# Kernel optimization log

Measured on AMD Instinct MI355X. Metric: run time of the kernel, lower is better.

Reference implementation:

```python
import jax, jax.numpy as jnp
import numpy as np
from jax import lax

B, T, E = 2, 2048, 2048
H, D = 16, 128
C = H * D          # qk_dim == v_dim == 2048
K = 4              # short conv kernel size
EPS = 1e-5


def setup_inputs() -> dict:
    key = jax.random.key(0)
    ks = jax.random.split(key, 11)
    s = 0.02
    return {
        "x": jax.random.normal(ks[0], (B, T, E), dtype=jnp.float32),
        "recurrent_state": jnp.zeros((B, H, D, D), dtype=jnp.float32),
        "Wq": jax.random.normal(ks[1], (C, E), dtype=jnp.float32) * s,
        "Wk": jax.random.normal(ks[2], (C, E), dtype=jnp.float32) * s,
        "Wv": jax.random.normal(ks[3], (C, E), dtype=jnp.float32) * s,
        "Wbeta": jax.random.normal(ks[4], (H, E), dtype=jnp.float32) * s,
        "Wgate": jax.random.normal(ks[5], (C, E), dtype=jnp.float32) * s,
        "Wo": jax.random.normal(ks[6], (E, C), dtype=jnp.float32) * s,
        "wq_conv": jax.random.normal(ks[7], (C, 1, K), dtype=jnp.float32) * 0.5,
        "wk_conv": jax.random.normal(ks[8], (C, 1, K), dtype=jnp.float32) * 0.5,
        "wv_conv": jax.random.normal(ks[9], (C, 1, K), dtype=jnp.float32) * 0.5,
    }


def _causal_dwconv(u, w):
    # u: (B, T, C), w: (C, 1, K). Torch pads both sides by K-1 then truncates
    # to length T -> equivalent to causal left-pad of K-1.
    u = u.transpose(0, 2, 1)  # (B, C, T)
    y = lax.conv_general_dilated(
        u, w, window_strides=(1,), padding=[(K - 1, 0)],
        feature_group_count=C, dimension_numbers=("NCH", "OIH", "NCH"))
    return y.transpose(0, 2, 1)  # (B, T, C)


def _delta_scan(q, k, v, beta, state):
    # q,k,v: (B,T,H,D); beta: (B,T,H); state: (B,H,D,D)
    def step(S, inp):
        qt, kt, vt, bt = inp  # (B,H,D),(B,H,D),(B,H,D),(B,H)
        b = bt[..., None, None]
        S = (1.0 - b) * S + b * (kt[..., :, None] * vt[..., None, :])  # bhde
        o = jnp.einsum("bhde,bhd->bhe", S, qt)
        return S, o

    xs = (q.transpose(1, 0, 2, 3), k.transpose(1, 0, 2, 3),
          v.transpose(1, 0, 2, 3), beta.transpose(1, 0, 2))
    final_state, outs = lax.scan(step, state, xs)
    return outs.transpose(1, 0, 2, 3), final_state  # (B,T,H,D)


def reference(x, recurrent_state, Wq, Wk, Wv, Wbeta, Wgate, Wo,
              wq_conv, wk_conv, wv_conv):
    q = jax.nn.silu(_causal_dwconv(x @ Wq.T, wq_conv))
    k = jax.nn.silu(_causal_dwconv(x @ Wk.T, wk_conv))
    v = jax.nn.silu(_causal_dwconv(x @ Wv.T, wv_conv))
    beta = jax.nn.sigmoid(x @ Wbeta.T)   # (B,T,H)
    gate = jax.nn.sigmoid(x @ Wgate.T)   # (B,T,C)

    q = q.reshape(B, T, H, D) * (D ** -0.5)
    k = k.reshape(B, T, H, D)
    v = v.reshape(B, T, H, D)

    out, new_state = _delta_scan(q, k, v, beta, recurrent_state)  # (B,T,H,D)

    # GroupNorm(num_groups=H, channels=C, affine=False) over (B, C, T):
    # normalizes each (batch, head) group over its (D, T) elements.
    mean = out.mean(axis=(1, 3), keepdims=True)
    var = out.var(axis=(1, 3), keepdims=True)
    out = (out - mean) * lax.rsqrt(var + EPS)

    out = out.reshape(B, T, C) * gate
    y = out @ Wo.T  # (B,T,E)
    return y, new_state
```

## Files before the change

### kernel.cpp

```cpp
#include <hip/hip_runtime.h>
#include <hip/hip_bf16.h>
#include <math.h>

#define BB 2
#define TT 2048
#define EE 2048
#define HH 16
#define DD 128
#define CC 2048
#define KCONV 4
#define CHUNK 128
#define NC 16
#define GN_EPS 1e-5f

typedef __bf16 bf16x8 __attribute__((ext_vector_type(8)));
typedef __bf16 bf16x4 __attribute__((ext_vector_type(4)));
typedef float  f32x4  __attribute__((ext_vector_type(4)));

#define GLD16(gp, lp)                                                          \
  __builtin_amdgcn_global_load_lds(                                            \
      (const __attribute__((address_space(1))) void*)(gp),                     \
      (__attribute__((address_space(3))) void*)(lp), 16, 0, 0)

__device__ __forceinline__ bf16x8 ldfrag(const __bf16* buf, int row, int kg)
{
  return *(const bf16x8*)(buf + row * 128 + ((kg ^ (row & 7)) << 3));
}

__global__ __launch_bounds__(256)
void convert_all(const float* __restrict__ x,  const float* __restrict__ Wq,
                 const float* __restrict__ Wk, const float* __restrict__ Wv,
                 const float* __restrict__ Wg, const float* __restrict__ Wo,
                 __bf16* __restrict__ xbf, __bf16* __restrict__ Wcat,
                 __bf16* __restrict__ Wob)
{
  const int i = (blockIdx.x * 256 + threadIdx.x) * 4;
  const int XN = 8388608, WN = 4194304;
  const float* src;
  __bf16* dst;
  int off;
  if (i < XN) { src = x; dst = xbf; off = i; }
  else if (i < XN + 4 * WN) {
    const int j = i - XN;
    const int seg = j >> 22;
    src = seg == 0 ? Wq : seg == 1 ? Wk : seg == 2 ? Wv : Wg;
    dst = Wcat + ((size_t)seg << 22);
    off = j & (WN - 1);
  } else { src = Wo; dst = Wob; off = i - XN - 4 * WN; }
  const float4 v = *(const float4*)(src + off);
  bf16x4 o;
  o[0] = (__bf16)v.x; o[1] = (__bf16)v.y; o[2] = (__bf16)v.z; o[3] = (__bf16)v.w;
  *(bf16x4*)(dst + off) = o;
}

__global__ __launch_bounds__(256)
void beta_ker(const float* __restrict__ x, const float* __restrict__ Wb,
              float* __restrict__ betab)
{
  __shared__ float wsb[16 * 1024];
  const int tid = threadIdx.x;
  const int w = tid >> 6, lane = tid & 63;
  const int row = blockIdx.x * 4 + w;
  const float* xrow = x + (size_t)row * EE;

  float acc[16] = {};
#pragma unroll
  for (int kt = 0; kt < 2; ++kt) {
    __syncthreads();
#pragma unroll
    for (int it = 0; it < 16; ++it) {
      const int i = tid + it * 256;
      const int h = i >> 8, kq = i & 255;
      *(float4*)&wsb[h * 1024 + kq * 4] =
          *(const float4*)(Wb + (size_t)h * EE + kt * 1024 + kq * 4);
    }
    __syncthreads();
#pragma unroll
    for (int j = 0; j < 4; ++j) {
      const int kof = lane * 4 + j * 256;
      const float4 xv = *(const float4*)(xrow + kt * 1024 + kof);
#pragma unroll
      for (int h = 0; h < 16; ++h) {
        const float4 wv = *(const float4*)&wsb[h * 1024 + kof];
        acc[h] += xv.x * wv.x + xv.y * wv.y + xv.z * wv.z + xv.w * wv.w;
      }
    }
  }
#pragma unroll
  for (int h = 0; h < 16; ++h) {
#pragma unroll
    for (int off = 32; off; off >>= 1)
      acc[h] += __shfl_xor(acc[h], off, 64);
  }
#pragma unroll
  for (int h = 0; h < 16; ++h)
    if (lane == h)
      betab[(size_t)row * HH + h] = 1.f / (1.f + expf(-acc[h]));
}

__global__ __launch_bounds__(512)
void gemm_big(const __bf16* __restrict__ A, const __bf16* __restrict__ Bm,
              __bf16* __restrict__ o0, __bf16* __restrict__ o1,
              __bf16* __restrict__ o2, __bf16* __restrict__ o3)
{
  __shared__ __attribute__((aligned(16))) unsigned char smem[163840];
  __bf16 (*ldsA)[256 * 64] = (__bf16(*)[256 * 64])smem;
  __bf16 (*ldsB)[256 * 64] = (__bf16(*)[256 * 64])(smem + 98304);

  const int tid = threadIdx.x;
  const int w = tid >> 6, l = tid & 63;
  const int wm = w >> 2, wn = w & 3;
  const int m0 = blockIdx.y * 256, n0 = blockIdx.x * 256;
  const int NT = EE / 64;

  const int sr0 = w * 8 + (l >> 3);
  const int skg = l & 7;
  const int fr = l & 15;
  const int fkg = l >> 4;

#define STAGE_A(tile, half) do {                                               \
    const int b_ = (tile) % 3;                                                 \
    const int r0_ = sr0;                                                       \
    const int r1_ = 64 + sr0;                                                  \
    GLD16(A + (size_t)(m0 + (half) * 128 + r0_) * 2048 + (tile) * 64           \
              + ((skg ^ (r0_ & 7)) << 3),                                      \
          ldsA[b_] + ((half) * 128 + w * 8) * 64);                             \
    GLD16(A + (size_t)(m0 + (half) * 128 + r1_) * 2048 + (tile) * 64           \
              + ((skg ^ (r1_ & 7)) << 3),                                      \
          ldsA[b_] + ((half) * 128 + 64 + w * 8) * 64);                        \
  } while (0)

#define STAGE_B(tile, half) do {                                               \
    const int b_ = (tile) & 1;                                                 \
    const int r0_ = sr0;                                                       \
    const int r1_ = 64 + sr0;                                                  \
    GLD16(Bm + (size_t)(n0 + (half) * 128 + r0_) * 2048 + (tile) * 64          \
              + ((skg ^ (r0_ & 7)) << 3),                                      \
          ldsB[b_] + ((half) * 128 + w * 8) * 64);                             \
    GLD16(Bm + (size_t)(n0 + (half) * 128 + r1_) * 2048 + (tile) * 64          \
              + ((skg ^ (r1_ & 7)) << 3),                                      \
          ldsB[b_] + ((half) * 128 + 64 + w * 8) * 64);                        \
  } while (0)

#define LDA_FRAG(dst, ab, q, mf, ks) do {                                      \
    const int row_ = wm * 128 + (q) * 32 + (mf) * 16 + fr;                     \
    const int kg_ = (ks) * 4 + fkg;                                            \
    dst = *(const bf16x8*)&ldsA[ab][row_ * 64 + ((kg_ ^ (row_ & 7)) << 3)];    \
  } while (0)
#define LDB_FRAG(dst, bb, nf, ks) do {                                         \
    const int row_ = wn * 64 + (nf) * 16 + fr;                                 \
    const int kg_ = (ks) * 4 + fkg;                                            \
    dst = *(const bf16x8*)&ldsB[bb][row_ * 64 + ((kg_ ^ (row_ & 7)) << 3)];    \
  } while (0)

  f32x4 acc[8][4] = {};

  STAGE_A(0, 0); STAGE_A(0, 1); STAGE_B(0, 0); STAGE_B(0, 1);
  STAGE_A(1, 0); STAGE_A(1, 1); STAGE_B(1, 0);
  asm volatile("s_waitcnt vmcnt(6)" ::: "memory");
  __builtin_amdgcn_s_barrier();

  for (int t = 0; t < NT; ++t) {
    const int abuf = t % 3;
    const int bbuf = t & 1;
    bf16x8 bfr[4][2];

    {
#pragma unroll
      for (int nf = 0; nf < 4; ++nf)
#pragma unroll
        for (int ks = 0; ks < 2; ++ks) LDB_FRAG(bfr[nf][ks], bbuf, nf, ks);
      bf16x8 af[2][2];
#pragma unroll
      for (int mf = 0; mf < 2; ++mf)
#pragma unroll
        for (int ks = 0; ks < 2; ++ks) LDA_FRAG(af[mf][ks], abuf, 0, mf, ks);
      if (t + 1 < NT) STAGE_B(t + 1, 1);
      __builtin_amdgcn_s_barrier();
      __builtin_amdgcn_s_setprio(1);
#pragma unroll
      for (int mf = 0; mf < 2; ++mf)
#pragma unroll
        for (int nf = 0; nf < 4; ++nf)
#pragma unroll
          for (int ks = 0; ks < 2; ++ks)
            acc[mf][nf] = __builtin_amdgcn_mfma_f32_16x16x32_bf16(
                af[mf][ks], bfr[nf][ks], acc[mf][nf], 0, 0, 0);
      __builtin_amdgcn_s_setprio(0);
    }

#pragma unroll
    for (int q = 1; q < 4; ++q) {
      bf16x8 af[2][2];
#pragma unroll
      for (int mf = 0; mf < 2; ++mf)
#pragma unroll
        for (int ks = 0; ks < 2; ++ks) LDA_FRAG(af[mf][ks], abuf, q, mf, ks);
      if (q == 1) {
        if (t + 2 < NT) STAGE_A(t + 2, 0);
      } else if (q == 2) {
        if (t + 2 < NT) STAGE_A(t + 2, 1);
      } else {
        if (t + 2 < NT) STAGE_B(t + 2, 0);
        if (t == NT - 2)     asm volatile("s_waitcnt vmcnt(0)" ::: "memory");
        else if (t < NT - 2) asm volatile("s_waitcnt vmcnt(6)" ::: "memory");
      }
      __builtin_amdgcn_s_barrier();
      __builtin_amdgcn_s_setprio(1);
#pragma unroll
      for (int mf = 0; mf < 2; ++mf)
#pragma unroll
        for (int nf = 0; nf < 4; ++nf)
#pragma unroll
          for (int ks = 0; ks < 2; ++ks)
            acc[2 * q + mf][nf] = __builtin_amdgcn_mfma_f32_16x16x32_bf16(
                af[mf][ks], bfr[nf][ks], acc[2 * q + mf][nf], 0, 0, 0);
      __builtin_amdgcn_s_setprio(0);
    }
  }

  __syncthreads();
  const int proj = n0 >> 11;
  const int nb = n0 & 2047;
  __bf16* outp = proj == 0 ? o0 : proj == 1 ? o1 : proj == 2 ? o2 : o3;
  __bf16* ep = (__bf16*)smem + (size_t)w * 9216;
  const int crow = (l >> 4) * 4;
#pragma unroll
  for (int mf2 = 0; mf2 < 8; ++mf2)
#pragma unroll
    for (int nf = 0; nf < 4; ++nf)
#pragma unroll
      for (int r = 0; r < 4; ++r) {
        const int row = mf2 * 16 + crow + r;
        float vv = acc[mf2][nf][r];
        if (proj == 3) vv = 1.f / (1.f + expf(-vv));
        ep[row * 72 + nf * 16 + fr] = (__bf16)vv;
      }
#pragma unroll
  for (int it = 0; it < 16; ++it) {
    const int row = it * 8 + (l >> 3);
    const int c8 = (l & 7) * 8;
    const bf16x8 v8 = *(const bf16x8*)&ep[row * 72 + c8];
    *(bf16x8*)(outp + (size_t)(m0 + wm * 128 + row) * 2048 + nb + wn * 64 + c8) = v8;
  }
#undef STAGE_A
#undef STAGE_B
#undef LDA_FRAG
#undef LDB_FRAG
}

__global__ __launch_bounds__(512)
void gemm_wo(const __bf16* __restrict__ A, const __bf16* __restrict__ Bm,
             float* __restrict__ Cm)
{
  __shared__ __attribute__((aligned(16))) unsigned char smem[147456];
  __bf16 (*ldsA)[128 * 64] = (__bf16(*)[128 * 64])smem;
  __bf16 (*ldsB)[256 * 64] = (__bf16(*)[256 * 64])(smem + 49152);

  const int tid = threadIdx.x;
  const int w = tid >> 6, l = tid & 63;
  const int wm = w >> 2, wn = w & 3;
  const int m0 = blockIdx.y * 128, n0 = blockIdx.x * 256;
  const int NT = CC / 64;

  const int sr0 = w * 8 + (l >> 3);
  const int skg = l & 7;
  const int fr = l & 15;
  const int fkg = l >> 4;

#define STAGE_AW(tile) do {                                                    \
    const int b_ = (tile) % 3;                                                 \
    const int r0_ = sr0;                                                       \
    const int r1_ = 64 + sr0;                                                  \
    GLD16(A + (size_t)(m0 + r0_) * 2048 + (tile) * 64                          \
              + ((skg ^ (r0_ & 7)) << 3),                                      \
          ldsA[b_] + (w * 8) * 64);                                            \
    GLD16(A + (size_t)(m0 + r1_) * 2048 + (tile) * 64                          \
              + ((skg ^ (r1_ & 7)) << 3),                                      \
          ldsA[b_] + (64 + w * 8) * 64);                                       \
  } while (0)

#define STAGE_BW(tile, half) do {                                              \
    const int b_ = (tile) % 3;                                                 \
    const int r0_ = sr0;                                                       \
    const int r1_ = 64 + sr0;                                                  \
    GLD16(Bm + (size_t)(n0 + (half) * 128 + r0_) * 2048 + (tile) * 64          \
              + ((skg ^ (r0_ & 7)) << 3),                                      \
          ldsB[b_] + ((half) * 128 + w * 8) * 64);                             \
    GLD16(Bm + (size_t)(n0 + (half) * 128 + r1_) * 2048 + (tile) * 64          \
              + ((skg ^ (r1_ & 7)) << 3),                                      \
          ldsB[b_] + ((half) * 128 + 64 + w * 8) * 64);                        \
  } while (0)

#define LDA_FRAGW(dst, ab, mf, ks) do {                                        \
    const int row_ = wm * 64 + (mf) * 16 + fr;                                 \
    const int kg_ = (ks) * 4 + fkg;                                            \
    dst = *(const bf16x8*)&ldsA[ab][row_ * 64 + ((kg_ ^ (row_ & 7)) << 3)];    \
  } while (0)
#define LDB_FRAGW(dst, bb, nf, ks) do {                                        \
    const int row_ = wn * 64 + (nf) * 16 + fr;                                 \
    const int kg_ = (ks) * 4 + fkg;                                            \
    dst = *(const bf16x8*)&ldsB[bb][row_ * 64 + ((kg_ ^ (row_ & 7)) << 3)];    \
  } while (0)

  f32x4 acc[4][4] = {};

  STAGE_BW(0, 0); STAGE_BW(0, 1); STAGE_AW(0);
  STAGE_BW(1, 0); STAGE_BW(1, 1); STAGE_AW(1);
  asm volatile("s_waitcnt vmcnt(6)" ::: "memory");
  __builtin_amdgcn_s_barrier();

  for (int t = 0; t < NT; ++t) {
    const int buf = t % 3;
    bf16x8 bfr[4][2];
    bf16x8 af[2][2];

#pragma unroll
    for (int nf = 0; nf < 4; ++nf)
#pragma unroll
      for (int ks = 0; ks < 2; ++ks) LDB_FRAGW(bfr[nf][ks], buf, nf, ks);
#pragma unroll
    for (int mf = 0; mf < 2; ++mf)
#pragma unroll
      for (int ks = 0; ks < 2; ++ks) LDA_FRAGW(af[mf][ks], buf, mf, ks);
    if (t + 2 < NT) { STAGE_BW(t + 2, 0); STAGE_BW(t + 2, 1); }
    __builtin_amdgcn_s_barrier();
    __builtin_amdgcn_s_setprio(1);
#pragma unroll
    for (int mf = 0; mf < 2; ++mf)
#pragma unroll
      for (int nf = 0; nf < 4; ++nf)
#pragma unroll
        for (int ks = 0; ks < 2; ++ks)
          acc[mf][nf] = __builtin_amdgcn_mfma_f32_16x16x32_bf16(
              af[mf][ks], bfr[nf][ks], acc[mf][nf], 0, 0, 0);
    __builtin_amdgcn_s_setprio(0);

#pragma unroll
    for (int mf = 0; mf < 2; ++mf)
#pragma unroll
      for (int ks = 0; ks < 2; ++ks) LDA_FRAGW(af[mf][ks], buf, mf + 2, ks);
    if (t + 2 < NT) STAGE_AW(t + 2);
    if (t == NT - 2)     asm volatile("s_waitcnt vmcnt(0)" ::: "memory");
    else if (t < NT - 2) asm volatile("s_waitcnt vmcnt(6)" ::: "memory");
    __builtin_amdgcn_s_barrier();
    __builtin_amdgcn_s_setprio(1);
#pragma unroll
    for (int mf = 0; mf < 2; ++mf)
#pragma unroll
      for (int nf = 0; nf < 4; ++nf)
#pragma unroll
        for (int ks = 0; ks < 2; ++ks)
          acc[mf + 2][nf] = __builtin_amdgcn_mfma_f32_16x16x32_bf16(
              af[mf][ks], bfr[nf][ks], acc[mf + 2][nf], 0, 0, 0);
    __builtin_amdgcn_s_setprio(0);
  }

  __syncthreads();
  float* ep = (float*)smem + (size_t)w * (64 * 68);
  const int crow = (l >> 4) * 4;
#pragma unroll
  for (int mf = 0; mf < 4; ++mf)
#pragma unroll
    for (int nf = 0; nf < 4; ++nf)
#pragma unroll
      for (int r = 0; r < 4; ++r)
        ep[(mf * 16 + crow + r) * 68 + nf * 16 + fr] = acc[mf][nf][r];
#pragma unroll
  for (int it = 0; it < 16; ++it) {
    const int row = it * 4 + (l >> 4);
    const int c4 = (l & 15) * 4;
    const float4 v4 = *(const float4*)&ep[row * 68 + c4];
    *(float4*)(Cm + (size_t)(m0 + wm * 64 + row) * 2048 + n0 + wn * 64 + c4) = v4;
  }
#undef STAGE_AW
#undef STAGE_BW
#undef LDA_FRAGW
#undef LDB_FRAGW
}

__global__ __launch_bounds__(256)
void conv_tr(const __bf16* __restrict__ u_q, const __bf16* __restrict__ u_k,
             const __bf16* __restrict__ u_v, const float* __restrict__ wq,
             const float* __restrict__ wk, const float* __restrict__ wv,
             __bf16* __restrict__ qbf, __bf16* __restrict__ kbf,
             __bf16* __restrict__ kT, __bf16* __restrict__ vT, float qscale)
{
  const int t0 = blockIdx.x * 64, c0 = blockIdx.y * 64;
  const int which = blockIdx.z / BB, b = blockIdx.z % BB;
  const __bf16* u = which == 0 ? u_q : which == 1 ? u_k : u_v;
  const float* wc = which == 0 ? wq : which == 1 ? wk : wv;
  const float scale = which == 0 ? qscale : 1.f;
  const int tid = threadIdx.x;
  __shared__ __attribute__((aligned(16))) __bf16 tile[64][72];

#pragma unroll
  for (int it = 0; it < 2; ++it) {
    const int idx = tid + it * 256;
    const int tl = idx >> 3, g = idx & 7;
    const int t = t0 + tl;
    const int c8 = c0 + g * 8;
    const size_t base = ((size_t)(b * TT + t)) * CC + c8;
    const bf16x8 z = {};
    const bf16x8 uu0 = *(const bf16x8*)(u + base);
    const bf16x8 uu1 = (t >= 1) ? *(const bf16x8*)(u + base - CC)     : z;
    const bf16x8 uu2 = (t >= 2) ? *(const bf16x8*)(u + base - 2 * CC) : z;
    const bf16x8 uu3 = (t >= 3) ? *(const bf16x8*)(u + base - 3 * CC) : z;
    bf16x8 o;
#pragma unroll
    for (int jj = 0; jj < 8; ++jj) {
      const float4 wv4 = *(const float4*)(wc + (size_t)(c8 + jj) * 4);
      const float vv = wv4.x * (float)uu3[jj] + wv4.y * (float)uu2[jj]
                     + wv4.z * (float)uu1[jj] + wv4.w * (float)uu0[jj];
      o[jj] = (__bf16)(vv / (1.f + expf(-vv)) * scale);
    }
    if (which == 0) *(bf16x8*)(qbf + base) = o;
    if (which == 1) *(bf16x8*)(kbf + base) = o;
    if (which >= 1) *(bf16x8*)&tile[tl][g * 8] = o;
  }
  if (which >= 1) {
    __syncthreads();
    const int h = c0 >> 7, d0 = c0 & 127;
    const int bh = b * HH + h;
    __bf16* dst = (which == 1) ? kT : vT;
#pragma unroll
    for (int it = 0; it < 2; ++it) {
      const int idx = tid + it * 256;
      const int dl = idx >> 3, g = idx & 7;
      bf16x8 o;
#pragma unroll
      for (int jj = 0; jj < 8; ++jj) o[jj] = tile[g * 8 + jj][dl];
      *(bf16x8*)(dst + ((size_t)(bh * DD + d0 + dl)) * TT + t0 + g * 8) = o;
    }
  }
}

__global__ __launch_bounds__(256)
void tr_f32(const float* __restrict__ in, float* __restrict__ out)
{
  const int r0 = blockIdx.x * 64, c0 = blockIdx.y * 64;
  const int bh = blockIdx.z;
  const int tid = threadIdx.x;
  __shared__ float tile[64][65];

#pragma unroll
  for (int it = 0; it < 4; ++it) {
    const int idx = tid + it * 256;
    const int rl = idx >> 4, g = idx & 15;
    const float4 v = *(const float4*)(in + (size_t)bh * 16384 + (r0 + rl) * 128 + c0 + g * 4);
    tile[rl][g * 4 + 0] = v.x; tile[rl][g * 4 + 1] = v.y;
    tile[rl][g * 4 + 2] = v.z; tile[rl][g * 4 + 3] = v.w;
  }
  __syncthreads();
#pragma unroll
  for (int it = 0; it < 4; ++it) {
    const int idx = tid + it * 256;
    const int cl = idx >> 4, g = idx & 15;
    float4 o;
    o.x = tile[g * 4 + 0][cl]; o.y = tile[g * 4 + 1][cl];
    o.z = tile[g * 4 + 2][cl]; o.w = tile[g * 4 + 3][cl];
    *(float4*)(out + (size_t)bh * 16384 + (c0 + cl) * 128 + r0 + g * 4) = o;
  }
}

__global__ __launch_bounds__(256)
void phaseA_mfma(const __bf16* __restrict__ kT, const __bf16* __restrict__ vT,
                 const float* __restrict__ beta, float* __restrict__ contribT,
                 float* __restrict__ decay)
{
  const int c = blockIdx.x, h = blockIdx.y, b = blockIdx.z;
  const int bh = b * HH + h;
  const int tid = threadIdx.x;
  const int w = tid >> 6, lane = tid & 63;
  const int wm = w >> 1, wn = w & 1;

  __shared__ __attribute__((aligned(16))) __bf16 bufVT[128 * 128];
  __shared__ __attribute__((aligned(16))) __bf16 bufKW[128 * 128];
  __shared__ float lc[CHUNK], bsh[CHUNK], wgt[CHUNK];

  {
    const __bf16* vbase = vT + ((size_t)bh * DD) * TT + c * CHUNK;
#pragma unroll
    for (int jj = 0; jj < 8; ++jj) {
      const int row = w * 32 + jj * 4 + (lane >> 4);
      const int g = lane & 15;
      GLD16(vbase + (size_t)row * TT + ((g ^ (row & 7)) << 3),
            bufVT + (w * 32 + jj * 4) * 128);
    }
  }

  if (tid < CHUNK) {
    const float bv = beta[(size_t)(b * TT + c * CHUNK + tid) * HH + h];
    bsh[tid] = bv;
    lc[tid] = log1pf(-bv);
  }
  __syncthreads();
  for (int off = 1; off < CHUNK; off <<= 1) {
    float add = 0.f;
    if (tid < CHUNK && tid >= off) add = lc[tid - off];
    __syncthreads();
    if (tid < CHUNK) lc[tid] += add;
    __syncthreads();
  }
  const float lend = lc[CHUNK - 1];
  if (tid < CHUNK) wgt[tid] = bsh[tid] * expf(lend - lc[tid]);
  if (tid == 0) decay[(size_t)bh * NC + c] = expf(lend);
  __syncthreads();

  {
    const __bf16* kbase = kT + ((size_t)bh * DD) * TT + c * CHUNK;
#pragma unroll
    for (int it = 0; it < 8; ++it) {
      const int idx = tid + it * 256;
      const int d = idx >> 4, g = idx & 15;
      const bf16x8 kv = *(const bf16x8*)(kbase + (size_t)d * TT + g * 8);
      bf16x8 o;
#pragma unroll
      for (int jj = 0; jj < 8; ++jj)
        o[jj] = (__bf16)((float)kv[jj] * wgt[g * 8 + jj]);
      *(bf16x8*)(bufKW + d * 128 + ((g ^ (d & 7)) << 3)) = o;
    }
  }
  asm volatile("s_waitcnt vmcnt(0)" ::: "memory");
  __syncthreads();

  f32x4 acc[4][4] = {};
#pragma unroll
  for (int ks = 0; ks < 4; ++ks) {
    bf16x8 a[4], bq[4];
    const int kg = ks * 4 + (lane >> 4);
#pragma unroll
    for (int f = 0; f < 4; ++f) a[f]  = ldfrag(bufVT, wm * 64 + f * 16 + (lane & 15), kg);
#pragma unroll
    for (int f = 0; f < 4; ++f) bq[f] = ldfrag(bufKW, wn * 64 + f * 16 + (lane & 15), kg);
#pragma unroll
    for (int i = 0; i < 4; ++i)
#pragma unroll
      for (int j = 0; j < 4; ++j)
        acc[i][j] = __builtin_amdgcn_mfma_f32_16x16x32_bf16(a[i], bq[j], acc[i][j], 0, 0, 0);
  }

  float* cp = contribT + ((size_t)(bh * NC + c) << 14);
  const int crow = (lane >> 4) * 4;
#pragma unroll
  for (int i = 0; i < 4; ++i)
#pragma unroll
    for (int j = 0; j < 4; ++j) {
      const int dd = wn * 64 + j * 16 + (lane & 15);
#pragma unroll
      for (int r = 0; r < 4; ++r) {
        const int e = wm * 64 + i * 16 + crow + r;
        cp[(size_t)e * 128 + dd] = acc[i][j][r];
      }
    }
}

__global__ __launch_bounds__(256)
void phaseB_T(const float* __restrict__ state0T, const float* __restrict__ contribT,
              const float* __restrict__ decay, __bf16* __restrict__ statesT,
              float* __restrict__ stateOutT)
{
  const size_t gid = (size_t)blockIdx.x * 256 + threadIdx.x;
  const int bh = (int)(gid >> 14);
  float s = state0T[gid];
  const float* dc = decay + (size_t)bh * NC;
  const int ed = (int)(gid & 16383);
#pragma unroll
  for (int c = 0; c < NC; ++c) {
    const size_t off = ((size_t)(bh * NC + c) << 14) + ed;
    statesT[off] = (__bf16)s;
    s = fmaf(dc[c], s, contribT[off]);
  }
  stateOutT[gid] = s;
}

__global__ __launch_bounds__(256)
void phaseC_mfma(const __bf16* __restrict__ qb, const __bf16* __restrict__ kb,
                 const __bf16* __restrict__ vT, const float* __restrict__ beta,
                 const __bf16* __restrict__ statesT, float* __restrict__ att,
                 float* __restrict__ partials)
{
  const int c = blockIdx.x, h = blockIdx.y, b = blockIdx.z;
  const int bh = b * HH + h;
  const int tid = threadIdx.x;
  const int w = tid >> 6, lane = tid & 63;
  const int wm = w >> 1, wn = w & 1;

  __shared__ __attribute__((aligned(16))) __bf16 bufQ[128 * 128];
  __shared__ __attribute__((aligned(16))) __bf16 bufB[128 * 128];
  __shared__ float lc[CHUNK], bsh[CHUNK];
  __shared__ float s1[256], s2[256];

  {
    const __bf16* qbase = qb + ((size_t)(b * TT + c * CHUNK)) * CC + h * DD;
    const __bf16* kbase = kb + ((size_t)(b * TT + c * CHUNK)) * CC + h * DD;
#pragma unroll
    for (int jj = 0; jj < 8; ++jj) {
      const int row = w * 32 + jj * 4 + (lane >> 4);
      const int g = lane & 15;
      GLD16(qbase + (size_t)row * CC + ((g ^ (row & 7)) << 3),
            bufQ + (w * 32 + jj * 4) * 128);
      GLD16(kbase + (size_t)row * CC + ((g ^ (row & 7)) << 3),
            bufB + (w * 32 + jj * 4) * 128);
    }
  }

  if (tid < CHUNK) {
    const float bv = beta[(size_t)(b * TT + c * CHUNK + tid) * HH + h];
    bsh[tid] = bv;
    lc[tid] = log1pf(-bv);
  }
  __syncthreads();
  for (int off = 1; off < CHUNK; off <<= 1) {
    float add = 0.f;
    if (tid < CHUNK && tid >= off) add = lc[tid - off];
    __syncthreads();
    if (tid < CHUNK) lc[tid] += add;
    __syncthreads();
  }

  asm volatile("s_waitcnt vmcnt(0)" ::: "memory");
  __syncthreads();

  f32x4 accS[4][4] = {};
#pragma unroll
  for (int ks = 0; ks < 4; ++ks) {
    bf16x8 a[4], bq[4];
    const int kg = ks * 4 + (lane >> 4);
#pragma unroll
    for (int f = 0; f < 4; ++f) a[f]  = ldfrag(bufQ, wm * 64 + f * 16 + (lane & 15), kg);
#pragma unroll
    for (int f = 0; f < 4; ++f) bq[f] = ldfrag(bufB, wn * 64 + f * 16 + (lane & 15), kg);
#pragma unroll
    for (int i = 0; i < 4; ++i)
#pragma unroll
      for (int j = 0; j < 4; ++j)
        accS[i][j] = __builtin_amdgcn_mfma_f32_16x16x32_bf16(a[i], bq[j], accS[i][j], 0, 0, 0);
  }

  __syncthreads();
  {
    const __bf16* sbase = statesT + ((size_t)(bh * NC + c) << 14);
#pragma unroll
    for (int jj = 0; jj < 8; ++jj) {
      const int row = w * 32 + jj * 4 + (lane >> 4);
      const int g = lane & 15;
      GLD16(sbase + (size_t)row * 128 + ((g ^ (row & 7)) << 3),
            bufB + (w * 32 + jj * 4) * 128);
    }
  }
  asm volatile("s_waitcnt vmcnt(0)" ::: "memory");
  __syncthreads();

  f32x4 accO[4][4] = {};
#pragma unroll
  for (int ks = 0; ks < 4; ++ks) {
    bf16x8 a[4], bq[4];
    const int kg = ks * 4 + (lane >> 4);
#pragma unroll
    for (int f = 0; f < 4; ++f) a[f]  = ldfrag(bufQ, wm * 64 + f * 16 + (lane & 15), kg);
#pragma unroll
    for (int f = 0; f < 4; ++f) bq[f] = ldfrag(bufB, wn * 64 + f * 16 + (lane & 15), kg);
#pragma unroll
    for (int i = 0; i < 4; ++i)
#pragma unroll
      for (int j = 0; j < 4; ++j)
        accO[i][j] = __builtin_amdgcn_mfma_f32_16x16x32_bf16(a[i], bq[j], accO[i][j], 0, 0, 0);
  }
  const int crow = (lane >> 4) * 4;
#pragma unroll
  for (int i = 0; i < 4; ++i)
#pragma unroll
    for (int r = 0; r < 4; ++r) {
      const float el = expf(lc[wm * 64 + i * 16 + crow + r]);
#pragma unroll
      for (int j = 0; j < 4; ++j) accO[i][j][r] *= el;
    }

  __syncthreads();
  {
    const __bf16* vbase = vT + ((size_t)bh * DD) * TT + c * CHUNK;
#pragma unroll
    for (int jj = 0; jj < 8; ++jj) {
      const int row = w * 32 + jj * 4 + (lane >> 4);
      const int g = lane & 15;
      GLD16(vbase + (size_t)row * TT + ((g ^ (row & 7)) << 3),
            bufB + (w * 32 + jj * 4) * 128);
    }
  }
  {
    float lcs[4], bss[4];
#pragma unroll
    for (int j = 0; j < 4; ++j) {
      const int s = wn * 64 + j * 16 + (lane & 15);
      lcs[j] = lc[s]; bss[j] = bsh[s];
    }
#pragma unroll
    for (int i = 0; i < 4; ++i)
#pragma unroll
      for (int r = 0; r < 4; ++r) {
        const int t = wm * 64 + i * 16 + crow + r;
        const float lct = lc[t];
#pragma unroll
        for (int j = 0; j < 4; ++j) {
          const int s = wn * 64 + j * 16 + (lane & 15);
          float p = 0.f;
          if (s <= t) p = accS[i][j][r] * bss[j] * expf(lct - lcs[j]);
          bufQ[t * 128 + (((s >> 3) ^ (t & 7)) << 3) + (s & 7)] = (__bf16)p;
        }
      }
  }
  asm volatile("s_waitcnt vmcnt(0)" ::: "memory");
  __syncthreads();

#pragma unroll
  for (int ks = 0; ks < 4; ++ks) {
    bf16x8 a[4], bq[4];
    const int kg = ks * 4 + (lane >> 4);
#pragma unroll
    for (int f = 0; f < 4; ++f) a[f]  = ldfrag(bufQ, wm * 64 + f * 16 + (lane & 15), kg);
#pragma unroll
    for (int f = 0; f < 4; ++f) bq[f] = ldfrag(bufB, wn * 64 + f * 16 + (lane & 15), kg);
#pragma unroll
    for (int i = 0; i < 4; ++i)
#pragma unroll
      for (int j = 0; j < 4; ++j)
        accO[i][j] = __builtin_amdgcn_mfma_f32_16x16x32_bf16(a[i], bq[j], accO[i][j], 0, 0, 0);
  }

  float lsum = 0.f, lsq = 0.f;
  float* obase = att + ((size_t)(b * TT + c * CHUNK)) * CC + h * DD;
#pragma unroll
  for (int i = 0; i < 4; ++i)
#pragma unroll
    for (int j = 0; j < 4; ++j) {
      const int e = wn * 64 + j * 16 + (lane & 15);
#pragma unroll
      for (int r = 0; r < 4; ++r) {
        const int t = wm * 64 + i * 16 + crow + r;
        const float vv = accO[i][j][r];
        obase[(size_t)t * CC + e] = vv;
        lsum += vv;
        lsq  += vv * vv;
      }
    }
  s1[tid] = lsum; s2[tid] = lsq;
  __syncthreads();
  for (int off = 128; off; off >>= 1) {
    if (tid < off) { s1[tid] += s1[tid + off]; s2[tid] += s2[tid + off]; }
    __syncthreads();
  }
  if (tid == 0) {
    partials[(size_t)(bh * NC + c) * 2]     = s1[0];
    partials[(size_t)(bh * NC + c) * 2 + 1] = s2[0];
  }
}

__global__ __launch_bounds__(64)
void gn_combine(const float* __restrict__ partials, float* __restrict__ stats)
{
  const int bh = blockIdx.x;
  const int lane = threadIdx.x;
  float s = 0.f, q = 0.f;
  if (lane < NC) {
    s = partials[(size_t)(bh * NC + lane) * 2];
    q = partials[(size_t)(bh * NC + lane) * 2 + 1];
  }
#pragma unroll
  for (int off = 8; off; off >>= 1) {
    s += __shfl_xor(s, off, 64);
    q += __shfl_xor(q, off, 64);
  }
  if (lane == 0) {
    const float n = (float)(TT * DD);
    const float mean = s / n;
    const float var = q / n - mean * mean;
    stats[bh * 2] = mean;
    stats[bh * 2 + 1] = rsqrtf(var + GN_EPS);
  }
}

__global__ __launch_bounds__(256)
void norm_gate(const float* __restrict__ att, const __bf16* __restrict__ gate,
               const float* __restrict__ stats, __bf16* __restrict__ g)
{
  const size_t gid = ((size_t)blockIdx.x * 256 + threadIdx.x) * 4;
  if (gid >= (size_t)BB * TT * CC) return;
  const int cpos = (int)(gid % CC);
  const int b = (int)(gid / ((size_t)TT * CC));
  const int bh = b * HH + (cpos >> 7);
  const float mean = stats[bh * 2], rstd = stats[bh * 2 + 1];
  const float4 a = *(const float4*)(att + gid);
  const bf16x4 gt = *(const bf16x4*)(gate + gid);
  bf16x4 o;
  o[0] = (__bf16)((a.x - mean) * rstd * (float)gt[0]);
  o[1] = (__bf16)((a.y - mean) * rstd * (float)gt[1]);
  o[2] = (__bf16)((a.z - mean) * rstd * (float)gt[2]);
  o[3] = (__bf16)((a.w - mean) * rstd * (float)gt[3]);
  *(bf16x4*)(g + gid) = o;
}

extern "C" void kernel_launch(void* const* d_in, const int* in_sizes, int n_in,
                              void* d_out, int out_size, void* d_ws, size_t ws_size,
                              hipStream_t stream)
{
  const float* x      = (const float*)d_in[0];
  const float* st0    = (const float*)d_in[1];
  const float* Wq     = (const float*)d_in[2];
  const float* Wk     = (const float*)d_in[3];
  const float* Wv     = (const float*)d_in[4];
  const float* Wbeta  = (const float*)d_in[5];
  const float* Wgate  = (const float*)d_in[6];
  const float* Wo     = (const float*)d_in[7];
  const float* wqc    = (const float*)d_in[8];
  const float* wkc    = (const float*)d_in[9];
  const float* wvc    = (const float*)d_in[10];

  float* ws = (float*)d_ws;
  __bf16* qbf  = (__bf16*)(ws + 0);
  __bf16* kbf  = (__bf16*)(ws + 4194304);
  __bf16* u_v  = (__bf16*)(ws + 8388608);
  __bf16* statesT = (__bf16*)(ws + 8388608);
  __bf16* kT   = (__bf16*)(ws + 12582912);
  __bf16* gbf  = (__bf16*)(ws + 12582912);
  __bf16* vT   = (__bf16*)(ws + 16777216);
  __bf16* xbf  = (__bf16*)(ws + 20971520);
  float* contribT = ws + 20971520;
  __bf16* Wcat = (__bf16*)(ws + 25165824);
  __bf16* gatebuf = (__bf16*)(ws + 33554432);
  float* betab    = ws + 37748736;
  float* decay    = ws + 37814272;
  float* stats    = ws + 37814784;
  float* partials = ws + 37814848;
  float* state0T  = ws + 37815872;
  float* stateOutT= ws + 38340160;
  __bf16* Wob  = (__bf16*)(ws + 38864448);

  float* y_out  = (float*)d_out;
  float* st_out = (float*)d_out + (size_t)BB * TT * EE;
  __bf16* u_q = (__bf16*)d_out;
  __bf16* u_k = (__bf16*)d_out + 8388608;
  float* att = y_out;

  const dim3 blk(256);
  const dim3 gBig(8192 / 256, (BB * TT) / 256);
  const dim3 gWo(EE / 256, (BB * TT) / 128);
  const dim3 gConv(TT / 64, CC / 64, 3 * BB);
  const dim3 gTrS(2, 2, BB * HH);
  const dim3 gScan(NC, HH, BB);
  const float qscale = 0.08838834764831845f;

  convert_all<<<dim3(28672), blk, 0, stream>>>(x, Wq, Wk, Wv, Wgate, Wo,
                                               xbf, Wcat, Wob);

  beta_ker<<<dim3((BB * TT) / 4), blk, 0, stream>>>(x, Wbeta, betab);

  gemm_big<<<gBig, dim3(512), 0, stream>>>(xbf, Wcat, u_q, u_k, u_v, gatebuf);

  conv_tr<<<gConv, blk, 0, stream>>>(u_q, u_k, u_v, wqc, wkc, wvc,
                                     qbf, kbf, kT, vT, qscale);

  tr_f32<<<gTrS, blk, 0, stream>>>(st0, state0T);

  phaseA_mfma<<<gScan, blk, 0, stream>>>(kT, vT, betab, contribT, decay);
  phaseB_T<<<dim3((BB * HH * DD * DD) / 256), blk, 0, stream>>>(state0T, contribT, decay, statesT, stateOutT);
  tr_f32<<<gTrS, blk, 0, stream>>>(stateOutT, st_out);
  phaseC_mfma<<<gScan, blk, 0, stream>>>(qbf, kbf, vT, betab, statesT, att, partials);

  gn_combine<<<dim3(BB * HH), dim3(64), 0, stream>>>(partials, stats);
  norm_gate<<<dim3((BB * TT * CC) / (256 * 4)), blk, 0, stream>>>(att, gatebuf, stats, gbf);

  gemm_wo<<<gWo, dim3(512), 0, stream>>>(gbf, Wob, y_out);
}
```

Before: 332.9 us.

## Reschedule GEMM main loops, fold state transposes and GN stats into neighbors

Both GEMM main loops are restructured with fewer barriers per k-step: gemm_big issues two half-tile MFMA phases instead of four, and gemm_wo uses a single wait/barrier with all fragments loaded up front. The two tr_f32 launches are removed by having phaseB_T read and write the recurrent state through transposed indexing. gn_combine is folded into norm_gate, which reduces the per-head partials in shared memory. This cuts kernel launches and barrier stalls but holds more fragment registers live and makes phaseB access the state with a strided pattern.

```diff
diff --git a/kernel.cpp b/kernel.cpp
--- a/kernel.cpp
+++ b/kernel.cpp
@@ -164,59 +164,54 @@
     const int abuf = t % 3;
     const int bbuf = t & 1;
     bf16x8 bfr[4][2];
-
-    {
+    bf16x8 af[4][2];
+
+#pragma unroll
+    for (int nf = 0; nf < 4; ++nf)
+#pragma unroll
+      for (int ks = 0; ks < 2; ++ks) LDB_FRAG(bfr[nf][ks], bbuf, nf, ks);
+#pragma unroll
+    for (int q = 0; q < 2; ++q)
+#pragma unroll
+      for (int mf = 0; mf < 2; ++mf)
+#pragma unroll
+        for (int ks = 0; ks < 2; ++ks)
+          LDA_FRAG(af[q * 2 + mf][ks], abuf, q, mf, ks);
+    __builtin_amdgcn_s_barrier();
+    if (t + 1 < NT) STAGE_B(t + 1, 1);
+    if (t + 2 < NT) { STAGE_A(t + 2, 0); STAGE_A(t + 2, 1); }
+    __builtin_amdgcn_s_setprio(1);
+#pragma unroll
+    for (int m2 = 0; m2 < 4; ++m2)
 #pragma unroll
       for (int nf = 0; nf < 4; ++nf)
 #pragma unroll
-        for (int ks = 0; ks < 2; ++ks) LDB_FRAG(bfr[nf][ks], bbuf, nf, ks);
-      bf16x8 af[2][2];
+        for (int ks = 0; ks < 2; ++ks)
+          acc[m2][nf] = __builtin_amdgcn_mfma_f32_16x16x32_bf16(
+              af[m2][ks], bfr[nf][ks], acc[m2][nf], 0, 0, 0);
+    __builtin_amdgcn_s_setprio(0);
+
+#pragma unroll
+    for (int q = 0; q < 2; ++q)
 #pragma unroll
       for (int mf = 0; mf < 2; ++mf)
 #pragma unroll
-        for (int ks = 0; ks < 2; ++ks) LDA_FRAG(af[mf][ks], abuf, 0, mf, ks);
-      if (t + 1 < NT) STAGE_B(t + 1, 1);
-      __builtin_amdgcn_s_barrier();
-      __builtin_amdgcn_s_setprio(1);
-#pragma unroll
-      for (int mf = 0; mf < 2; ++mf)
-#pragma unroll
-        for (int nf = 0; nf < 4; ++nf)
-#pragma unroll
-          for (int ks = 0; ks < 2; ++ks)
-            acc[mf][nf] = __builtin_amdgcn_mfma_f32_16x16x32_bf16(
-                af[mf][ks], bfr[nf][ks], acc[mf][nf], 0, 0, 0);
-      __builtin_amdgcn_s_setprio(0);
-    }
-
-#pragma unroll
-    for (int q = 1; q < 4; ++q) {
-      bf16x8 af[2][2];
-#pragma unroll
-      for (int mf = 0; mf < 2; ++mf)
-#pragma unroll
-        for (int ks = 0; ks < 2; ++ks) LDA_FRAG(af[mf][ks], abuf, q, mf, ks);
-      if (q == 1) {
-        if (t + 2 < NT) STAGE_A(t + 2, 0);
-      } else if (q == 2) {
-        if (t + 2 < NT) STAGE_A(t + 2, 1);
-      } else {
-        if (t + 2 < NT) STAGE_B(t + 2, 0);
-        if (t == NT - 2)     asm volatile("s_waitcnt vmcnt(0)" ::: "memory");
-        else if (t < NT - 2) asm volatile("s_waitcnt vmcnt(6)" ::: "memory");
-      }
-      __builtin_amdgcn_s_barrier();
-      __builtin_amdgcn_s_setprio(1);
-#pragma unroll
-      for (int mf = 0; mf < 2; ++mf)
-#pragma unroll
-        for (int nf = 0; nf < 4; ++nf)
-#pragma unroll
-          for (int ks = 0; ks < 2; ++ks)
-            acc[2 * q + mf][nf] = __builtin_amdgcn_mfma_f32_16x16x32_bf16(
-                af[mf][ks], bfr[nf][ks], acc[2 * q + mf][nf], 0, 0, 0);
-      __builtin_amdgcn_s_setprio(0);
-    }
+        for (int ks = 0; ks < 2; ++ks)
+          LDA_FRAG(af[q * 2 + mf][ks], abuf, q + 2, mf, ks);
+    if (t == NT - 2)     asm volatile("s_waitcnt vmcnt(0)" ::: "memory");
+    else if (t < NT - 2) asm volatile("s_waitcnt vmcnt(4)" ::: "memory");
+    __builtin_amdgcn_s_barrier();
+    if (t + 2 < NT) STAGE_B(t + 2, 0);
+    __builtin_amdgcn_s_setprio(1);
+#pragma unroll
+    for (int m2 = 0; m2 < 4; ++m2)
+#pragma unroll
+      for (int nf = 0; nf < 4; ++nf)
+#pragma unroll
+        for (int ks = 0; ks < 2; ++ks)
+          acc[m2 + 4][nf] = __builtin_amdgcn_mfma_f32_16x16x32_bf16(
+              af[m2][ks], bfr[nf][ks], acc[m2 + 4][nf], 0, 0, 0);
+    __builtin_amdgcn_s_setprio(0);
   }
 
   __syncthreads();
@@ -307,52 +302,36 @@
 
   STAGE_BW(0, 0); STAGE_BW(0, 1); STAGE_AW(0);
   STAGE_BW(1, 0); STAGE_BW(1, 1); STAGE_AW(1);
-  asm volatile("s_waitcnt vmcnt(6)" ::: "memory");
-  __builtin_amdgcn_s_barrier();
 
   for (int t = 0; t < NT; ++t) {
     const int buf = t % 3;
     bf16x8 bfr[4][2];
-    bf16x8 af[2][2];
+    bf16x8 af[4][2];
+
+    if (t == NT - 1) asm volatile("s_waitcnt vmcnt(0)" ::: "memory");
+    else             asm volatile("s_waitcnt vmcnt(6)" ::: "memory");
+    __builtin_amdgcn_s_barrier();
 
 #pragma unroll
     for (int nf = 0; nf < 4; ++nf)
 #pragma unroll
       for (int ks = 0; ks < 2; ++ks) LDB_FRAGW(bfr[nf][ks], buf, nf, ks);
 #pragma unroll
-    for (int mf = 0; mf < 2; ++mf)
+    for (int mf = 0; mf < 4; ++mf)
 #pragma unroll
       for (int ks = 0; ks < 2; ++ks) LDA_FRAGW(af[mf][ks], buf, mf, ks);
-    if (t + 2 < NT) { STAGE_BW(t + 2, 0); STAGE_BW(t + 2, 1); }
-    __builtin_amdgcn_s_barrier();
+
+    if (t + 2 < NT) { STAGE_BW(t + 2, 0); STAGE_BW(t + 2, 1); STAGE_AW(t + 2); }
+
     __builtin_amdgcn_s_setprio(1);
 #pragma unroll
-    for (int mf = 0; mf < 2; ++mf)
+    for (int mf = 0; mf < 4; ++mf)
 #pragma unroll
       for (int nf = 0; nf < 4; ++nf)
 #pragma unroll
         for (int ks = 0; ks < 2; ++ks)
           acc[mf][nf] = __builtin_amdgcn_mfma_f32_16x16x32_bf16(
               af[mf][ks], bfr[nf][ks], acc[mf][nf], 0, 0, 0);
-    __builtin_amdgcn_s_setprio(0);
-
-#pragma unroll
-    for (int mf = 0; mf < 2; ++mf)
-#pragma unroll
-      for (int ks = 0; ks < 2; ++ks) LDA_FRAGW(af[mf][ks], buf, mf + 2, ks);
-    if (t + 2 < NT) STAGE_AW(t + 2);
-    if (t == NT - 2)     asm volatile("s_waitcnt vmcnt(0)" ::: "memory");
-    else if (t < NT - 2) asm volatile("s_waitcnt vmcnt(6)" ::: "memory");
-    __builtin_amdgcn_s_barrier();
-    __builtin_amdgcn_s_setprio(1);
-#pragma unroll
-    for (int mf = 0; mf < 2; ++mf)
-#pragma unroll
-      for (int nf = 0; nf < 4; ++nf)
-#pragma unroll
-        for (int ks = 0; ks < 2; ++ks)
-          acc[mf + 2][nf] = __builtin_amdgcn_mfma_f32_16x16x32_bf16(
-              af[mf][ks], bfr[nf][ks], acc[mf + 2][nf], 0, 0, 0);
     __builtin_amdgcn_s_setprio(0);
   }
 
@@ -436,34 +415,6 @@
 }
 
 __global__ __launch_bounds__(256)
-void tr_f32(const float* __restrict__ in, float* __restrict__ out)
-{
-  const int r0 = blockIdx.x * 64, c0 = blockIdx.y * 64;
-  const int bh = blockIdx.z;
-  const int tid = threadIdx.x;
-  __shared__ float tile[64][65];
-
-#pragma unroll
-  for (int it = 0; it < 4; ++it) {
-    const int idx = tid + it * 256;
-    const int rl = idx >> 4, g = idx & 15;
-    const float4 v = *(const float4*)(in + (size_t)bh * 16384 + (r0 + rl) * 128 + c0 + g * 4);
-    tile[rl][g * 4 + 0] = v.x; tile[rl][g * 4 + 1] = v.y;
-    tile[rl][g * 4 + 2] = v.z; tile[rl][g * 4 + 3] = v.w;
-  }
-  __syncthreads();
-#pragma unroll
-  for (int it = 0; it < 4; ++it) {
-    const int idx = tid + it * 256;
-    const int cl = idx >> 4, g = idx & 15;
-    float4 o;
-    o.x = tile[g * 4 + 0][cl]; o.y = tile[g * 4 + 1][cl];
-    o.z = tile[g * 4 + 2][cl]; o.w = tile[g * 4 + 3][cl];
-    *(float4*)(out + (size_t)bh * 16384 + (c0 + cl) * 128 + r0 + g * 4) = o;
-  }
-}
-
-__global__ __launch_bounds__(256)
 void phaseA_mfma(const __bf16* __restrict__ kT, const __bf16* __restrict__ vT,
                  const float* __restrict__ beta, float* __restrict__ contribT,
                  float* __restrict__ decay)
@@ -556,22 +507,24 @@
 }
 
 __global__ __launch_bounds__(256)
-void phaseB_T(const float* __restrict__ state0T, const float* __restrict__ contribT,
+void phaseB_T(const float* __restrict__ st0, const float* __restrict__ contribT,
               const float* __restrict__ decay, __bf16* __restrict__ statesT,
-              float* __restrict__ stateOutT)
+              float* __restrict__ stOut)
 {
   const size_t gid = (size_t)blockIdx.x * 256 + threadIdx.x;
   const int bh = (int)(gid >> 14);
-  float s = state0T[gid];
+  const int ed = (int)(gid & 16383);
+  const int e = ed >> 7, d = ed & 127;
+  const size_t tidx = ((size_t)bh << 14) + (size_t)d * 128 + e;
+  float s = st0[tidx];
   const float* dc = decay + (size_t)bh * NC;
-  const int ed = (int)(gid & 16383);
 #pragma unroll
   for (int c = 0; c < NC; ++c) {
     const size_t off = ((size_t)(bh * NC + c) << 14) + ed;
     statesT[off] = (__bf16)s;
     s = fmaf(dc[c], s, contribT[off]);
   }
-  stateOutT[gid] = s;
+  stOut[tidx] = s;
 }
 
 __global__ __launch_bounds__(256)
@@ -756,40 +709,32 @@
   }
 }
 
-__global__ __launch_bounds__(64)
-void gn_combine(const float* __restrict__ partials, float* __restrict__ stats)
-{
-  const int bh = blockIdx.x;
-  const int lane = threadIdx.x;
-  float s = 0.f, q = 0.f;
-  if (lane < NC) {
-    s = partials[(size_t)(bh * NC + lane) * 2];
-    q = partials[(size_t)(bh * NC + lane) * 2 + 1];
-  }
-#pragma unroll
-  for (int off = 8; off; off >>= 1) {
-    s += __shfl_xor(s, off, 64);
-    q += __shfl_xor(q, off, 64);
-  }
-  if (lane == 0) {
+__global__ __launch_bounds__(256)
+void norm_gate(const float* __restrict__ att, const __bf16* __restrict__ gate,
+               const float* __restrict__ partials, __bf16* __restrict__ g)
+{
+  __shared__ float sm[8], sr[8];
+  const int tid = threadIdx.x;
+  const size_t gid0 = (size_t)blockIdx.x * 1024;
+  const int b = (int)(gid0 >> 22);
+  const int h0 = ((int)(gid0 & 2047)) >> 7;
+  if (tid < 8) {
+    const int bh = b * HH + h0 + tid;
+    float s = 0.f, q = 0.f;
+#pragma unroll
+    for (int cc = 0; cc < NC; ++cc) {
+      s += partials[(size_t)(bh * NC + cc) * 2];
+      q += partials[(size_t)(bh * NC + cc) * 2 + 1];
+    }
     const float n = (float)(TT * DD);
     const float mean = s / n;
-    const float var = q / n - mean * mean;
-    stats[bh * 2] = mean;
-    stats[bh * 2 + 1] = rsqrtf(var + GN_EPS);
-  }
-}
-
-__global__ __launch_bounds__(256)
-void norm_gate(const float* __restrict__ att, const __bf16* __restrict__ gate,
-               const float* __restrict__ stats, __bf16* __restrict__ g)
-{
-  const size_t gid = ((size_t)blockIdx.x * 256 + threadIdx.x) * 4;
-  if (gid >= (size_t)BB * TT * CC) return;
-  const int cpos = (int)(gid % CC);
-  const int b = (int)(gid / ((size_t)TT * CC));
-  const int bh = b * HH + (cpos >> 7);
-  const float mean = stats[bh * 2], rstd = stats[bh * 2 + 1];
+    sm[tid] = mean;
+    sr[tid] = rsqrtf(q / n - mean * mean + GN_EPS);
+  }
+  __syncthreads();
+  const size_t gid = gid0 + (size_t)tid * 4;
+  const int hl = (tid * 4) >> 7;
+  const float mean = sm[hl], rstd = sr[hl];
   const float4 a = *(const float4*)(att + gid);
   const bf16x4 gt = *(const bf16x4*)(gate + gid);
   bf16x4 o;
@@ -830,10 +775,7 @@
   __bf16* gatebuf = (__bf16*)(ws + 33554432);
   float* betab    = ws + 37748736;
   float* decay    = ws + 37814272;
-  float* stats    = ws + 37814784;
   float* partials = ws + 37814848;
-  float* state0T  = ws + 37815872;
-  float* stateOutT= ws + 38340160;
   __bf16* Wob  = (__bf16*)(ws + 38864448);
 
   float* y_out  = (float*)d_out;
@@ -846,7 +788,6 @@
   const dim3 gBig(8192 / 256, (BB * TT) / 256);
   const dim3 gWo(EE / 256, (BB * TT) / 128);
   const dim3 gConv(TT / 64, CC / 64, 3 * BB);
-  const dim3 gTrS(2, 2, BB * HH);
   const dim3 gScan(NC, HH, BB);
   const float qscale = 0.08838834764831845f;
 
@@ -860,15 +801,11 @@
   conv_tr<<<gConv, blk, 0, stream>>>(u_q, u_k, u_v, wqc, wkc, wvc,
                                      qbf, kbf, kT, vT, qscale);
 
-  tr_f32<<<gTrS, blk, 0, stream>>>(st0, state0T);
-
   phaseA_mfma<<<gScan, blk, 0, stream>>>(kT, vT, betab, contribT, decay);
-  phaseB_T<<<dim3((BB * HH * DD * DD) / 256), blk, 0, stream>>>(state0T, contribT, decay, statesT, stateOutT);
-  tr_f32<<<gTrS, blk, 0, stream>>>(stateOutT, st_out);
+  phaseB_T<<<dim3((BB * HH * DD * DD) / 256), blk, 0, stream>>>(st0, contribT, decay, statesT, st_out);
   phaseC_mfma<<<gScan, blk, 0, stream>>>(qbf, kbf, vT, betab, statesT, att, partials);
 
-  gn_combine<<<dim3(BB * HH), dim3(64), 0, stream>>>(partials, stats);
-  norm_gate<<<dim3((BB * TT * CC) / (256 * 4)), blk, 0, stream>>>(att, gatebuf, stats, gbf);
+  norm_gate<<<dim3((BB * TT * CC) / 1024), blk, 0, stream>>>(att, gatebuf, partials, gbf);
 
   gemm_wo<<<gWo, dim3(512), 0, stream>>>(gbf, Wob, y_out);
 }
```

Result: no change. 333.0 us (+0.0%).
